# Performance work log

Measured on AMD Instinct MI355X. Metric: run time of the kernel, lower is better.

## Reference

```python
import jax, jax.numpy as jnp
import numpy as np

B, D = 8192, 64


def _mlp(x, w1, b1, w2, b2):
    # Linear -> exact GELU (torch nn.GELU default) -> Linear
    h = jax.nn.gelu(x @ w1 + b1, approximate=False)
    return h @ w2 + b2


def setup_inputs() -> dict:
    key = jax.random.key(0)
    ks = jax.random.split(key, 16)
    def lin(k, fan_in, fan_out):
        return jax.random.normal(k, (fan_in, fan_out), jnp.float32) / np.sqrt(fan_in).astype(np.float32)
    inp = {"z": jax.random.normal(ks[0], (B, 81, D), jnp.float32)}
    for i, name in enumerate(["row", "col", "box"]):
        inp[f"{name}_w1"] = lin(ks[1 + 4 * i], 9 * D, D)
        inp[f"{name}_b1"] = jnp.zeros((D,), jnp.float32)
        inp[f"{name}_w2"] = lin(ks[2 + 4 * i], D, D)
        inp[f"{name}_b2"] = jnp.zeros((D,), jnp.float32)
    inp["gate_w"] = lin(ks[13], 3 * D, D)
    inp["gate_b"] = jnp.zeros((D,), jnp.float32)
    inp["alpha"] = jnp.float32(0.1)
    return inp


def reference(z, row_w1, row_b1, row_w2, row_b2,
              col_w1, col_b1, col_w2, col_b2,
              box_w1, box_b1, box_w2, box_b2,
              gate_w, gate_b, alpha):
    Bv = z.shape[0]
    z_grid = z.reshape(Bv, 9, 9, D)
    # row context: each of 9 rows flattened -> (B, 9, 9D)
    row_ctx = z_grid.reshape(Bv, 9, 9 * D)
    row_up = _mlp(row_ctx, row_w1, row_b1, row_w2, row_b2)[:, :, None, :]  # (B,9,1,D)
    # col context: transpose rows/cols then flatten -> (B, 9, 9D)
    col_ctx = jnp.transpose(z_grid, (0, 2, 1, 3)).reshape(Bv, 9, 9 * D)
    col_up = _mlp(col_ctx, col_w1, col_b1, col_w2, col_b2)[:, None, :, :]  # (B,1,9,D)
    # box context: (B,3,3,3,3,D) -> (B, br, bc, r, c, D) -> (B, 9, 9D)
    box_ctx = jnp.transpose(z_grid.reshape(Bv, 3, 3, 3, 3, D), (0, 1, 3, 2, 4, 5)).reshape(Bv, 9, 9 * D)
    box_up = _mlp(box_ctx, box_w1, box_b1, box_w2, box_b2).reshape(Bv, 3, 3, D)
    # replicate exact torch expand+reshape semantics (mixes d and inner-col axes)
    box_up = jnp.broadcast_to(box_up[:, :, :, None, :, None], (Bv, 3, 3, 3, D, 3)).reshape(Bv, 9, 9, D)
    row_upb = jnp.broadcast_to(row_up, (Bv, 9, 9, D))
    col_upb = jnp.broadcast_to(col_up, (Bv, 9, 9, D))
    delta_sum = row_upb + col_upb + box_up
    gate_in = jnp.concatenate([row_upb, col_upb, box_up], axis=-1)  # (B,9,9,3D)
    gate = jax.nn.sigmoid(gate_in @ gate_w + gate_b)  # (B,9,9,D)
    z_new = z_grid + alpha * gate * delta_sum
    return z_new.reshape(Bv, 81, D)
```

## Files before the change

### kernel.cpp

```cpp
#include <hip/hip_runtime.h>
#include <hip/hip_bf16.h>

typedef __attribute__((ext_vector_type(8))) short short8;
typedef __attribute__((ext_vector_type(4))) short short4v;
typedef __attribute__((ext_vector_type(4))) float f32x4;

__device__ __forceinline__ unsigned short f2bf(float f) {
    union { __hip_bfloat16 b; unsigned short u; } v;
    v.b = __float2bfloat16(f);
    return v.u;
}
__device__ __forceinline__ float bf2f(unsigned short u) {
    return __uint_as_float(((unsigned)u) << 16);
}
__device__ __forceinline__ float gelu_tanh(float x) {
    float u = 0.79788456080286536f * x * (1.0f + 0.044715f * x * x);
    return x * __builtin_amdgcn_rcpf(1.0f + __builtin_exp2f(-2.8853900817779268f * u));
}
__device__ __forceinline__ float sigmoidf(float x) {
    return __builtin_amdgcn_rcpf(1.0f + __builtin_exp2f(-1.4426950408889634f * x));
}
__device__ __forceinline__ int swz(int row, int col) {
    return (row * 64 + col) ^ ((row & 7) << 3);
}

__global__ __launch_bounds__(256)
void prepack_kernel(const float* __restrict__ w1r, const float* __restrict__ w1c,
                    const float* __restrict__ w1b,
                    const float* __restrict__ w2r, const float* __restrict__ w2c,
                    const float* __restrict__ w2b,
                    const float* __restrict__ gw, unsigned short* __restrict__ ws)
{
    int t = blockIdx.x * 256 + threadIdx.x;
    if (t < 13824) {
        int wi = t / 4608, r = t % 4608;
        const float* src = (wi == 0) ? w1r : (wi == 1) ? w1c : w1b;
        unsigned short* dst = ws + wi * 36864;
        int lane = r & 63;
        int col = ((r >> 6) & 3) * 16 + (lane & 15);
        int k0 = (r >> 8) * 32 + (lane >> 4) * 8;
        #pragma unroll
        for (int j = 0; j < 8; ++j) dst[r * 8 + j] = f2bf(src[(k0 + j) * 64 + col]);
    } else if (t < 15360) {
        int q = t - 13824, wi = q / 512, r = q % 512;
        const float* src = (wi == 0) ? w2r : (wi == 1) ? w2c : w2b;
        unsigned short* dst = ws + 110592 + wi * 4096;
        int lane = r & 63;
        int col = ((r >> 6) & 3) * 16 + (lane & 15);
        int k0 = (r >> 8) * 32 + (lane >> 4) * 8;
        #pragma unroll
        for (int j = 0; j < 8; ++j) dst[r * 8 + j] = f2bf(src[(k0 + j) * 64 + col]);
    } else if (t < 17920) {
        int r = t - 15360;
        unsigned short* dst = ws + 122880;
        int lane = r & 63;
        int col = ((r >> 6) & 3) * 16 + (lane & 15);
        int k0 = (r >> 8) * 32 + (lane >> 4) * 8;
        #pragma unroll
        for (int j = 0; j < 8; ++j) {
            int krow = k0 + j;
            float v;
            if (krow < 128) {
                v = gw[krow * 64 + col];
            } else {
                int c = (krow - 128) >> 6, e = (krow - 128) & 63;
                int lo = 3 * e - 64 * c;
                v = 0.f;
                #pragma unroll
                for (int s = 0; s < 3; ++s) {
                    int dp = lo + s;
                    if (dp >= 0 && dp < 64) v += gw[(128 + dp) * 64 + col];
                }
            }
            dst[r * 8 + j] = f2bf(v);
        }
    }
}

#define UPWS_OFF 147456

__global__ __launch_bounds__(576, 2)
void k1_mlp(const float* __restrict__ z,
            const float* __restrict__ b1r, const float* __restrict__ b2r,
            const float* __restrict__ b1c, const float* __restrict__ b2c,
            const float* __restrict__ b1b, const float* __restrict__ b2b,
            const short* __restrict__ wsp, unsigned short* __restrict__ upws)
{
    __shared__ __align__(16) unsigned short zl[20736];
    __shared__ __align__(16) unsigned short hlds[9216];
    const int t = threadIdx.x;
    const int lane = t & 63;
    const int w = t >> 6;
    const int rl = lane & 15;
    const int kg = lane >> 4;
    const int b0 = blockIdx.x * 4;
    const int hoff = w * 1024;

    {
        const float* src = z + (size_t)b0 * 5184;
        #pragma unroll
        for (int it = 0; it < 9; ++it) {
            int g = t + it * 576;
            float4 v = *(const float4*)(src + g * 4);
            int row = g >> 4;
            int col = (g & 15) * 4;
            uint2 pk;
            pk.x = ((unsigned)f2bf(v.y) << 16) | f2bf(v.x);
            pk.y = ((unsigned)f2bf(v.w) << 16) | f2bf(v.z);
            *(uint2*)&zl[swz(row, col)] = pk;
        }
    }
    __syncthreads();

    const int type = w / 3, pg = w % 3;
    const int b = rl & 3, js = rl >> 2;
    const int jraw = 4 * pg + js;
    const int j = (jraw < 9) ? jraw : 8;
    const int cellbase = (type == 0) ? j * 9
                       : (type == 1) ? j
                       :               (j / 3) * 27 + (j % 3) * 3;
    const int rowbase = b * 81 + cellbase;

    const short* w1p = wsp + type * 36864;
    const short* w2p = wsp + 110592 + type * 4096;
    const float* b1p = (type == 0) ? b1r : (type == 1) ? b1c : b1b;
    const float* b2p = (type == 0) ? b2r : (type == 1) ? b2c : b2b;
    float b1v[4], b2v[4];
    #pragma unroll
    for (int nt = 0; nt < 4; ++nt) { b1v[nt] = b1p[nt * 16 + rl]; b2v[nt] = b2p[nt * 16 + rl]; }

    f32x4 acc[4];
    #pragma unroll
    for (int nt = 0; nt < 4; ++nt) acc[nt] = (f32x4)0.f;

    #pragma unroll
    for (int kk = 0; kk < 18; ++kk) {
        const int s = kk >> 1;
        const int sadd = (type == 0) ? s : (type == 1) ? 9 * s : (s / 3) * 9 + (s % 3);
        const int feat = (kk & 1) * 32 + kg * 8;
        short8 a = *(const short8*)&zl[swz(rowbase + sadd, feat)];
        #pragma unroll
        for (int nt = 0; nt < 4; ++nt) {
            short8 bv = *(const short8*)(w1p + ((kk * 4 + nt) * 64 + lane) * 8);
            acc[nt] = __builtin_amdgcn_mfma_f32_16x16x32_bf16(a, bv, acc[nt], 0, 0, 0);
        }
    }

    #pragma unroll
    for (int nt = 0; nt < 4; ++nt)
        #pragma unroll
        for (int reg = 0; reg < 4; ++reg)
            hlds[hoff + swz(kg * 4 + reg, nt * 16 + rl)] =
                f2bf(gelu_tanh(acc[nt][reg] + b1v[nt]));
    asm volatile("s_waitcnt lgkmcnt(0)" ::: "memory");

    f32x4 a2c[4];
    #pragma unroll
    for (int nt = 0; nt < 4; ++nt) a2c[nt] = (f32x4)0.f;
    #pragma unroll
    for (int kk2 = 0; kk2 < 2; ++kk2) {
        short8 a2 = *(const short8*)&hlds[hoff + swz(rl, kk2 * 32 + kg * 8)];
        #pragma unroll
        for (int nt = 0; nt < 4; ++nt) {
            short8 bw = *(const short8*)(w2p + ((kk2 * 4 + nt) * 64 + lane) * 8);
            a2c[nt] = __builtin_amdgcn_mfma_f32_16x16x32_bf16(a2, bw, a2c[nt], 0, 0, 0);
        }
    }
    asm volatile("s_waitcnt lgkmcnt(0)" ::: "memory");
    #pragma unroll
    for (int nt = 0; nt < 4; ++nt)
        #pragma unroll
        for (int reg = 0; reg < 4; ++reg)
            hlds[hoff + swz(kg * 4 + reg, nt * 16 + rl)] = f2bf(a2c[nt][reg] + b2v[nt]);
    asm volatile("s_waitcnt lgkmcnt(0)" ::: "memory");

    #pragma unroll
    for (int p2 = 0; p2 < 2; ++p2) {
        const int hrow = p2 * 8 + (lane >> 3), f0 = (lane & 7) * 8;
        const int sjs = hrow >> 2, sb = hrow & 3;
        const int sj = 4 * pg + sjs;
        if (sj < 9) {
            short8 v = *(const short8*)&hlds[hoff + swz(hrow, f0)];
            *(short8*)(upws + ((size_t)(b0 + sb) * 27 + type * 9 + sj) * 64 + f0) = v;
        }
    }
}

__global__ __launch_bounds__(576, 4)
void k2_gate(const float* __restrict__ z, const unsigned short* __restrict__ upws,
             const short* __restrict__ wsp, const float* __restrict__ gb,
             const float* __restrict__ alphap, float* __restrict__ out)
{
    __shared__ __align__(16) unsigned short ups[27648];
    __shared__ __align__(16) unsigned short tscr[9][1024];
    const int t = threadIdx.x;
    const int lane = t & 63;
    const int w = t >> 6;
    const int rl = lane & 15;
    const int kg = lane >> 4;
    const int b0 = blockIdx.x * 16;

    #pragma unroll
    for (int c6 = 0; c6 < 6; ++c6) {
        int chunk = t + c6 * 576;
        int row = chunk >> 3, f0 = (chunk & 7) * 8;
        short8 v = *(const short8*)(upws + (size_t)b0 * 1728 + chunk * 8);
        *(short8*)&ups[swz(row, f0)] = v;
    }
    __syncthreads();

    const short* gwp = wsp + 122880;
    const float alpha = alphap[0];
    float gbl[4][4];
    #pragma unroll
    for (int mt = 0; mt < 4; ++mt)
        #pragma unroll
        for (int reg = 0; reg < 4; ++reg) gbl[mt][reg] = gb[mt * 16 + kg * 4 + reg];

    const int c = w % 3, wg = w / 3;

    #pragma unroll
    for (int tl = 0; tl < 9; ++tl) {
        int e = (wg * 9 + tl) * 16 + rl;
        int b = e / 27, rem = e % 27, R = rem / 3, q = rem % 3, C = c + 3 * q;
        int rowR = b * 27 + R, rowC = b * 27 + 9 + C, rowB = b * 27 + 18 + R;

        f32x4 acc[4];
        #pragma unroll
        for (int mt = 0; mt < 4; ++mt) acc[mt] = (f32x4)0.f;

        #pragma unroll
        for (int s6 = 0; s6 < 6; ++s6) {
            int seg = s6 >> 1;
            int kkp = (s6 < 4) ? s6 : 4 + 2 * c + (s6 - 4);
            int row = (seg == 0) ? rowR : (seg == 1) ? rowC : rowB;
            int f = (s6 & 1) * 32 + kg * 8;
            short8 bfrag = *(const short8*)&ups[swz(row, f)];
            #pragma unroll
            for (int mt = 0; mt < 4; ++mt) {
                short8 afrag = *(const short8*)(gwp + ((kkp * 4 + mt) * 64 + lane) * 8);
                acc[mt] = __builtin_amdgcn_mfma_f32_16x16x32_bf16(afrag, bfrag, acc[mt], 0, 0, 0);
            }
        }

        #pragma unroll
        for (int mt = 0; mt < 4; ++mt) {
            short4v du4 = *(const short4v*)&ups[swz(rowR, mt * 16 + kg * 4)];
            short4v dc4 = *(const short4v*)&ups[swz(rowC, mt * 16 + kg * 4)];
            #pragma unroll
            for (int reg = 0; reg < 4; ++reg) {
                int fidx = mt * 16 + kg * 4 + reg;
                float g = sigmoidf(acc[mt][reg] + gbl[mt][reg]);
                float duv = bf2f((unsigned short)du4[reg]);
                float dcv = bf2f((unsigned short)dc4[reg]);
                float dbv = bf2f(ups[swz(rowB, (64 * c + fidx) / 3)]);
                tscr[w][swz(rl, fidx)] = f2bf(alpha * g * (duv + dcv + dbv));
            }
        }
        asm volatile("s_waitcnt lgkmcnt(0)" ::: "memory");
        #pragma unroll
        for (int p = 0; p < 2; ++p) {
            int cl = p * 8 + (lane >> 3), f0 = (lane & 7) * 8;
            int e2 = (wg * 9 + tl) * 16 + cl;
            int b2 = e2 / 27, rem2 = e2 % 27, R2 = rem2 / 3, C2 = c + 3 * (rem2 % 3);
            short8 tv = *(const short8*)&tscr[w][swz(cl, f0)];
            const float* zp = z + (size_t)(b0 + b2) * 5184 + (size_t)(R2 * 9 + C2) * 64 + f0;
            float4 z0 = *(const float4*)zp;
            float4 z1 = *(const float4*)(zp + 4);
            float4 o0, o1;
            o0.x = z0.x + bf2f((unsigned short)tv[0]);
            o0.y = z0.y + bf2f((unsigned short)tv[1]);
            o0.z = z0.z + bf2f((unsigned short)tv[2]);
            o0.w = z0.w + bf2f((unsigned short)tv[3]);
            o1.x = z1.x + bf2f((unsigned short)tv[4]);
            o1.y = z1.y + bf2f((unsigned short)tv[5]);
            o1.z = z1.z + bf2f((unsigned short)tv[6]);
            o1.w = z1.w + bf2f((unsigned short)tv[7]);
            float* op = out + (size_t)(b0 + b2) * 5184 + (size_t)(R2 * 9 + C2) * 64 + f0;
            *(float4*)op = o0;
            *(float4*)(op + 4) = o1;
        }
        asm volatile("s_waitcnt lgkmcnt(0)" ::: "memory");
    }
}

extern "C" void kernel_launch(void* const* d_in, const int* in_sizes, int n_in,
                              void* d_out, int out_size, void* d_ws, size_t ws_size,
                              hipStream_t stream) {
    const float* z   = (const float*)d_in[0];
    const float* w1r = (const float*)d_in[1];
    const float* b1r = (const float*)d_in[2];
    const float* w2r = (const float*)d_in[3];
    const float* b2r = (const float*)d_in[4];
    const float* w1c = (const float*)d_in[5];
    const float* b1c = (const float*)d_in[6];
    const float* w2c = (const float*)d_in[7];
    const float* b2c = (const float*)d_in[8];
    const float* w1b = (const float*)d_in[9];
    const float* b1b = (const float*)d_in[10];
    const float* w2b = (const float*)d_in[11];
    const float* b2b = (const float*)d_in[12];
    const float* gw  = (const float*)d_in[13];
    const float* gb  = (const float*)d_in[14];
    const float* al  = (const float*)d_in[15];
    float* outp = (float*)d_out;
    unsigned short* ws = (unsigned short*)d_ws;

    prepack_kernel<<<70, 256, 0, stream>>>(w1r, w1c, w1b, w2r, w2c, w2b, gw, ws);

    const int Btot = in_sizes[0] / 5184;
    unsigned short* upws = ws + UPWS_OFF;
    k1_mlp<<<Btot / 4, 576, 0, stream>>>(z, b1r, b2r, b1c, b2c, b1b, b2b,
                                         (const short*)ws, upws);
    k2_gate<<<Btot / 16, 576, 0, stream>>>(z, upws, (const short*)ws, gb, al, outp);
}
```

Before: 184.8 us.

## Fuse MLP and gate kernels into one kernel keeping updates in LDS

Merges the two-kernel pipeline (MLP writing bf16 row/col/box updates to a global workspace, then a gate kernel reading them back) into a single kernel per 4-batch block. The updates stay in shared memory and the gate stage reuses the hlds scratch, dropping the workspace round-trip and one launch. In exchange the gate stage now runs with 12 of 16 MFMA rows active per tile and at the MLP kernel's lower occupancy bound of 2 blocks. LDS use per block also grows.

```diff
diff --git a/kernel.cpp b/kernel.cpp
--- a/kernel.cpp
+++ b/kernel.cpp
@@ -77,16 +77,17 @@
     }
 }
 
-#define UPWS_OFF 147456
-
 __global__ __launch_bounds__(576, 2)
-void k1_mlp(const float* __restrict__ z,
-            const float* __restrict__ b1r, const float* __restrict__ b2r,
-            const float* __restrict__ b1c, const float* __restrict__ b2c,
-            const float* __restrict__ b1b, const float* __restrict__ b2b,
-            const short* __restrict__ wsp, unsigned short* __restrict__ upws)
+void fused_kernel(const float* __restrict__ z,
+                  const float* __restrict__ b1r, const float* __restrict__ b2r,
+                  const float* __restrict__ b1c, const float* __restrict__ b2c,
+                  const float* __restrict__ b1b, const float* __restrict__ b2b,
+                  const float* __restrict__ gb, const float* __restrict__ alphap,
+                  const short* __restrict__ wsp,
+                  float* __restrict__ out)
 {
     __shared__ __align__(16) unsigned short zl[20736];
+    __shared__ __align__(16) unsigned short ups[6912];
     __shared__ __align__(16) unsigned short hlds[9216];
     const int t = threadIdx.x;
     const int lane = t & 63;
@@ -112,175 +113,161 @@
     }
     __syncthreads();
 
-    const int type = w / 3, pg = w % 3;
-    const int b = rl & 3, js = rl >> 2;
-    const int jraw = 4 * pg + js;
-    const int j = (jraw < 9) ? jraw : 8;
-    const int cellbase = (type == 0) ? j * 9
-                       : (type == 1) ? j
-                       :               (j / 3) * 27 + (j % 3) * 3;
-    const int rowbase = b * 81 + cellbase;
-
-    const short* w1p = wsp + type * 36864;
-    const short* w2p = wsp + 110592 + type * 4096;
-    const float* b1p = (type == 0) ? b1r : (type == 1) ? b1c : b1b;
-    const float* b2p = (type == 0) ? b2r : (type == 1) ? b2c : b2b;
-    float b1v[4], b2v[4];
-    #pragma unroll
-    for (int nt = 0; nt < 4; ++nt) { b1v[nt] = b1p[nt * 16 + rl]; b2v[nt] = b2p[nt * 16 + rl]; }
-
-    f32x4 acc[4];
-    #pragma unroll
-    for (int nt = 0; nt < 4; ++nt) acc[nt] = (f32x4)0.f;
-
-    #pragma unroll
-    for (int kk = 0; kk < 18; ++kk) {
-        const int s = kk >> 1;
-        const int sadd = (type == 0) ? s : (type == 1) ? 9 * s : (s / 3) * 9 + (s % 3);
-        const int feat = (kk & 1) * 32 + kg * 8;
-        short8 a = *(const short8*)&zl[swz(rowbase + sadd, feat)];
-        #pragma unroll
-        for (int nt = 0; nt < 4; ++nt) {
-            short8 bv = *(const short8*)(w1p + ((kk * 4 + nt) * 64 + lane) * 8);
-            acc[nt] = __builtin_amdgcn_mfma_f32_16x16x32_bf16(a, bv, acc[nt], 0, 0, 0);
-        }
-    }
-
-    #pragma unroll
-    for (int nt = 0; nt < 4; ++nt)
-        #pragma unroll
-        for (int reg = 0; reg < 4; ++reg)
-            hlds[hoff + swz(kg * 4 + reg, nt * 16 + rl)] =
-                f2bf(gelu_tanh(acc[nt][reg] + b1v[nt]));
-    asm volatile("s_waitcnt lgkmcnt(0)" ::: "memory");
-
-    f32x4 a2c[4];
-    #pragma unroll
-    for (int nt = 0; nt < 4; ++nt) a2c[nt] = (f32x4)0.f;
-    #pragma unroll
-    for (int kk2 = 0; kk2 < 2; ++kk2) {
-        short8 a2 = *(const short8*)&hlds[hoff + swz(rl, kk2 * 32 + kg * 8)];
-        #pragma unroll
-        for (int nt = 0; nt < 4; ++nt) {
-            short8 bw = *(const short8*)(w2p + ((kk2 * 4 + nt) * 64 + lane) * 8);
-            a2c[nt] = __builtin_amdgcn_mfma_f32_16x16x32_bf16(a2, bw, a2c[nt], 0, 0, 0);
-        }
-    }
-    asm volatile("s_waitcnt lgkmcnt(0)" ::: "memory");
-    #pragma unroll
-    for (int nt = 0; nt < 4; ++nt)
-        #pragma unroll
-        for (int reg = 0; reg < 4; ++reg)
-            hlds[hoff + swz(kg * 4 + reg, nt * 16 + rl)] = f2bf(a2c[nt][reg] + b2v[nt]);
-    asm volatile("s_waitcnt lgkmcnt(0)" ::: "memory");
-
-    #pragma unroll
-    for (int p2 = 0; p2 < 2; ++p2) {
-        const int hrow = p2 * 8 + (lane >> 3), f0 = (lane & 7) * 8;
-        const int sjs = hrow >> 2, sb = hrow & 3;
-        const int sj = 4 * pg + sjs;
-        if (sj < 9) {
-            short8 v = *(const short8*)&hlds[hoff + swz(hrow, f0)];
-            *(short8*)(upws + ((size_t)(b0 + sb) * 27 + type * 9 + sj) * 64 + f0) = v;
-        }
-    }
-}
-
-__global__ __launch_bounds__(576, 4)
-void k2_gate(const float* __restrict__ z, const unsigned short* __restrict__ upws,
-             const short* __restrict__ wsp, const float* __restrict__ gb,
-             const float* __restrict__ alphap, float* __restrict__ out)
-{
-    __shared__ __align__(16) unsigned short ups[27648];
-    __shared__ __align__(16) unsigned short tscr[9][1024];
-    const int t = threadIdx.x;
-    const int lane = t & 63;
-    const int w = t >> 6;
-    const int rl = lane & 15;
-    const int kg = lane >> 4;
-    const int b0 = blockIdx.x * 16;
-
-    #pragma unroll
-    for (int c6 = 0; c6 < 6; ++c6) {
-        int chunk = t + c6 * 576;
-        int row = chunk >> 3, f0 = (chunk & 7) * 8;
-        short8 v = *(const short8*)(upws + (size_t)b0 * 1728 + chunk * 8);
-        *(short8*)&ups[swz(row, f0)] = v;
+    {
+        const int type = w / 3, pg = w % 3;
+        const int b = rl & 3, js = rl >> 2;
+        const int jraw = 4 * pg + js;
+        const int j = (jraw < 9) ? jraw : 8;
+        const int cellbase = (type == 0) ? j * 9
+                           : (type == 1) ? j
+                           :               (j / 3) * 27 + (j % 3) * 3;
+        const int rowbase = b * 81 + cellbase;
+
+        const short* w1p = wsp + type * 36864;
+        const short* w2p = wsp + 110592 + type * 4096;
+        const float* b1p = (type == 0) ? b1r : (type == 1) ? b1c : b1b;
+        const float* b2p = (type == 0) ? b2r : (type == 1) ? b2c : b2b;
+        float b1v[4], b2v[4];
+        #pragma unroll
+        for (int nt = 0; nt < 4; ++nt) { b1v[nt] = b1p[nt * 16 + rl]; b2v[nt] = b2p[nt * 16 + rl]; }
+
+        f32x4 acc[4];
+        #pragma unroll
+        for (int nt = 0; nt < 4; ++nt) acc[nt] = (f32x4)0.f;
+
+        #pragma unroll
+        for (int kk = 0; kk < 18; ++kk) {
+            const int s = kk >> 1;
+            const int sadd = (type == 0) ? s : (type == 1) ? 9 * s : (s / 3) * 9 + (s % 3);
+            const int feat = (kk & 1) * 32 + kg * 8;
+            short8 a = *(const short8*)&zl[swz(rowbase + sadd, feat)];
+            #pragma unroll
+            for (int nt = 0; nt < 4; ++nt) {
+                short8 bv = *(const short8*)(w1p + ((kk * 4 + nt) * 64 + lane) * 8);
+                acc[nt] = __builtin_amdgcn_mfma_f32_16x16x32_bf16(a, bv, acc[nt], 0, 0, 0);
+            }
+        }
+
+        #pragma unroll
+        for (int nt = 0; nt < 4; ++nt)
+            #pragma unroll
+            for (int reg = 0; reg < 4; ++reg)
+                hlds[hoff + swz(kg * 4 + reg, nt * 16 + rl)] =
+                    f2bf(gelu_tanh(acc[nt][reg] + b1v[nt]));
+        asm volatile("s_waitcnt lgkmcnt(0)" ::: "memory");
+
+        f32x4 a2c[4];
+        #pragma unroll
+        for (int nt = 0; nt < 4; ++nt) a2c[nt] = (f32x4)0.f;
+        #pragma unroll
+        for (int kk2 = 0; kk2 < 2; ++kk2) {
+            short8 a2 = *(const short8*)&hlds[hoff + swz(rl, kk2 * 32 + kg * 8)];
+            #pragma unroll
+            for (int nt = 0; nt < 4; ++nt) {
+                short8 bw = *(const short8*)(w2p + ((kk2 * 4 + nt) * 64 + lane) * 8);
+                a2c[nt] = __builtin_amdgcn_mfma_f32_16x16x32_bf16(a2, bw, a2c[nt], 0, 0, 0);
+            }
+        }
+        asm volatile("s_waitcnt lgkmcnt(0)" ::: "memory");
+        #pragma unroll
+        for (int nt = 0; nt < 4; ++nt)
+            #pragma unroll
+            for (int reg = 0; reg < 4; ++reg)
+                hlds[hoff + swz(kg * 4 + reg, nt * 16 + rl)] = f2bf(a2c[nt][reg] + b2v[nt]);
+        asm volatile("s_waitcnt lgkmcnt(0)" ::: "memory");
+
+        #pragma unroll
+        for (int p2 = 0; p2 < 2; ++p2) {
+            const int hrow = p2 * 8 + (lane >> 3), f0 = (lane & 7) * 8;
+            const int sjs = hrow >> 2, sb = hrow & 3;
+            const int sj = 4 * pg + sjs;
+            if (sj < 9) {
+                short8 v = *(const short8*)&hlds[hoff + swz(hrow, f0)];
+                *(short8*)&ups[swz(sb * 27 + type * 9 + sj, f0)] = v;
+            }
+        }
     }
     __syncthreads();
 
-    const short* gwp = wsp + 122880;
-    const float alpha = alphap[0];
-    float gbl[4][4];
-    #pragma unroll
-    for (int mt = 0; mt < 4; ++mt)
-        #pragma unroll
-        for (int reg = 0; reg < 4; ++reg) gbl[mt][reg] = gb[mt * 16 + kg * 4 + reg];
-
-    const int c = w % 3, wg = w / 3;
-
-    #pragma unroll
-    for (int tl = 0; tl < 9; ++tl) {
-        int e = (wg * 9 + tl) * 16 + rl;
-        int b = e / 27, rem = e % 27, R = rem / 3, q = rem % 3, C = c + 3 * q;
-        int rowR = b * 27 + R, rowC = b * 27 + 9 + C, rowB = b * 27 + 18 + R;
-
-        f32x4 acc[4];
-        #pragma unroll
-        for (int mt = 0; mt < 4; ++mt) acc[mt] = (f32x4)0.f;
-
-        #pragma unroll
-        for (int s6 = 0; s6 < 6; ++s6) {
-            int seg = s6 >> 1;
-            int kkp = (s6 < 4) ? s6 : 4 + 2 * c + (s6 - 4);
-            int row = (seg == 0) ? rowR : (seg == 1) ? rowC : rowB;
-            int f = (s6 & 1) * 32 + kg * 8;
-            short8 bfrag = *(const short8*)&ups[swz(row, f)];
+    {
+        const short* gwp = wsp + 122880;
+        const float alpha = alphap[0];
+        float gbl[4][4];
+        #pragma unroll
+        for (int mt = 0; mt < 4; ++mt)
+            #pragma unroll
+            for (int reg = 0; reg < 4; ++reg) gbl[mt][reg] = gb[mt * 16 + kg * 4 + reg];
+
+        const int c = w % 3, wg = w / 3;
+
+        #pragma unroll
+        for (int ti = 0; ti < 3; ++ti) {
+            const int ebase = wg * 36 + ti * 12;
+            const int el = (rl < 12) ? rl : 11;
+            int e = ebase + el;
+            int b = e / 27, rem = e % 27, R = rem / 3, q = rem % 3, C = c + 3 * q;
+            int rowR = b * 27 + R, rowC = b * 27 + 9 + C, rowB = b * 27 + 18 + R;
+
+            f32x4 acc[4];
+            #pragma unroll
+            for (int mt = 0; mt < 4; ++mt) acc[mt] = (f32x4)0.f;
+
+            #pragma unroll
+            for (int s6 = 0; s6 < 6; ++s6) {
+                int seg = s6 >> 1;
+                int kkp = (s6 < 4) ? s6 : 4 + 2 * c + (s6 - 4);
+                int row = (seg == 0) ? rowR : (seg == 1) ? rowC : rowB;
+                int f = (s6 & 1) * 32 + kg * 8;
+                short8 bfrag = *(const short8*)&ups[swz(row, f)];
+                #pragma unroll
+                for (int mt = 0; mt < 4; ++mt) {
+                    short8 afrag = *(const short8*)(gwp + ((kkp * 4 + mt) * 64 + lane) * 8);
+                    acc[mt] = __builtin_amdgcn_mfma_f32_16x16x32_bf16(afrag, bfrag, acc[mt], 0, 0, 0);
+                }
+            }
+
             #pragma unroll
             for (int mt = 0; mt < 4; ++mt) {
-                short8 afrag = *(const short8*)(gwp + ((kkp * 4 + mt) * 64 + lane) * 8);
-                acc[mt] = __builtin_amdgcn_mfma_f32_16x16x32_bf16(afrag, bfrag, acc[mt], 0, 0, 0);
-            }
-        }
-
-        #pragma unroll
-        for (int mt = 0; mt < 4; ++mt) {
-            short4v du4 = *(const short4v*)&ups[swz(rowR, mt * 16 + kg * 4)];
-            short4v dc4 = *(const short4v*)&ups[swz(rowC, mt * 16 + kg * 4)];
-            #pragma unroll
-            for (int reg = 0; reg < 4; ++reg) {
-                int fidx = mt * 16 + kg * 4 + reg;
-                float g = sigmoidf(acc[mt][reg] + gbl[mt][reg]);
-                float duv = bf2f((unsigned short)du4[reg]);
-                float dcv = bf2f((unsigned short)dc4[reg]);
-                float dbv = bf2f(ups[swz(rowB, (64 * c + fidx) / 3)]);
-                tscr[w][swz(rl, fidx)] = f2bf(alpha * g * (duv + dcv + dbv));
-            }
-        }
-        asm volatile("s_waitcnt lgkmcnt(0)" ::: "memory");
-        #pragma unroll
-        for (int p = 0; p < 2; ++p) {
-            int cl = p * 8 + (lane >> 3), f0 = (lane & 7) * 8;
-            int e2 = (wg * 9 + tl) * 16 + cl;
-            int b2 = e2 / 27, rem2 = e2 % 27, R2 = rem2 / 3, C2 = c + 3 * (rem2 % 3);
-            short8 tv = *(const short8*)&tscr[w][swz(cl, f0)];
-            const float* zp = z + (size_t)(b0 + b2) * 5184 + (size_t)(R2 * 9 + C2) * 64 + f0;
-            float4 z0 = *(const float4*)zp;
-            float4 z1 = *(const float4*)(zp + 4);
-            float4 o0, o1;
-            o0.x = z0.x + bf2f((unsigned short)tv[0]);
-            o0.y = z0.y + bf2f((unsigned short)tv[1]);
-            o0.z = z0.z + bf2f((unsigned short)tv[2]);
-            o0.w = z0.w + bf2f((unsigned short)tv[3]);
-            o1.x = z1.x + bf2f((unsigned short)tv[4]);
-            o1.y = z1.y + bf2f((unsigned short)tv[5]);
-            o1.z = z1.z + bf2f((unsigned short)tv[6]);
-            o1.w = z1.w + bf2f((unsigned short)tv[7]);
-            float* op = out + (size_t)(b0 + b2) * 5184 + (size_t)(R2 * 9 + C2) * 64 + f0;
-            *(float4*)op = o0;
-            *(float4*)(op + 4) = o1;
-        }
-        asm volatile("s_waitcnt lgkmcnt(0)" ::: "memory");
+                short4v du4 = *(const short4v*)&ups[swz(rowR, mt * 16 + kg * 4)];
+                short4v dc4 = *(const short4v*)&ups[swz(rowC, mt * 16 + kg * 4)];
+                #pragma unroll
+                for (int reg = 0; reg < 4; ++reg) {
+                    int fidx = mt * 16 + kg * 4 + reg;
+                    float g = sigmoidf(acc[mt][reg] + gbl[mt][reg]);
+                    float duv = bf2f((unsigned short)du4[reg]);
+                    float dcv = bf2f((unsigned short)dc4[reg]);
+                    float dbv = bf2f(ups[swz(rowB, (64 * c + fidx) / 3)]);
+                    hlds[hoff + swz(rl, fidx)] = f2bf(alpha * g * (duv + dcv + dbv));
+                }
+            }
+            asm volatile("s_waitcnt lgkmcnt(0)" ::: "memory");
+
+            #pragma unroll
+            for (int p = 0; p < 2; ++p) {
+                int cl = p * 8 + (lane >> 3), f0 = (lane & 7) * 8;
+                if (cl < 12) {
+                    int e2 = ebase + cl;
+                    int b2 = e2 / 27, rem2 = e2 % 27, R2 = rem2 / 3, C2 = c + 3 * (rem2 % 3);
+                    short8 tv = *(const short8*)&hlds[hoff + swz(cl, f0)];
+                    const float* zp = z + (size_t)(b0 + b2) * 5184 + (size_t)(R2 * 9 + C2) * 64 + f0;
+                    float4 z0 = *(const float4*)zp;
+                    float4 z1 = *(const float4*)(zp + 4);
+                    float4 o0, o1;
+                    o0.x = z0.x + bf2f((unsigned short)tv[0]);
+                    o0.y = z0.y + bf2f((unsigned short)tv[1]);
+                    o0.z = z0.z + bf2f((unsigned short)tv[2]);
+                    o0.w = z0.w + bf2f((unsigned short)tv[3]);
+                    o1.x = z1.x + bf2f((unsigned short)tv[4]);
+                    o1.y = z1.y + bf2f((unsigned short)tv[5]);
+                    o1.z = z1.z + bf2f((unsigned short)tv[6]);
+                    o1.w = z1.w + bf2f((unsigned short)tv[7]);
+                    float* op = out + (size_t)(b0 + b2) * 5184 + (size_t)(R2 * 9 + C2) * 64 + f0;
+                    *(float4*)op = o0;
+                    *(float4*)(op + 4) = o1;
+                }
+            }
+            asm volatile("s_waitcnt lgkmcnt(0)" ::: "memory");
+        }
     }
 }
 
@@ -309,8 +296,6 @@
     prepack_kernel<<<70, 256, 0, stream>>>(w1r, w1c, w1b, w2r, w2c, w2b, gw, ws);
 
     const int Btot = in_sizes[0] / 5184;
-    unsigned short* upws = ws + UPWS_OFF;
-    k1_mlp<<<Btot / 4, 576, 0, stream>>>(z, b1r, b2r, b1c, b2c, b1b, b2b,
-                                         (const short*)ws, upws);
-    k2_gate<<<Btot / 16, 576, 0, stream>>>(z, upws, (const short*)ws, gb, al, outp);
-}
+    fused_kernel<<<Btot / 4, 576, 0, stream>>>(
+        z, b1r, b2r, b1c, b2c, b1b, b2b, gb, al, (const short*)ws, outp);
+}
```

Result: slower. 203.5 us (+10.1%).

## Repartition first MLP GEMM across 12 waves by output column quarter

Applied to the files above, without the earlier changes.

The first-layer GEMM in k1_mlp is remapped so that each of 12 waves (768 threads) owns one MLP type and one 16-column quarter of the output, and computes three row groups. Each weight fragment loaded from global memory is then reused across three MFMAs instead of one, with three A-fragment LDS reads per step. The second layer keeps the old 9-wave mapping and runs after a block-wide barrier. In exchange the block is larger, there is an extra __syncthreads, and three waves sit idle during the second layer.

```diff
diff --git a/kernel.cpp b/kernel.cpp
--- a/kernel.cpp
+++ b/kernel.cpp
@@ -79,7 +79,7 @@
 
 #define UPWS_OFF 147456
 
-__global__ __launch_bounds__(576, 2)
+__global__ __launch_bounds__(768, 2)
 void k1_mlp(const float* __restrict__ z,
             const float* __restrict__ b1r, const float* __restrict__ b2r,
             const float* __restrict__ b1c, const float* __restrict__ b2c,
@@ -94,13 +94,10 @@
     const int rl = lane & 15;
     const int kg = lane >> 4;
     const int b0 = blockIdx.x * 4;
-    const int hoff = w * 1024;
 
     {
         const float* src = z + (size_t)b0 * 5184;
-        #pragma unroll
-        for (int it = 0; it < 9; ++it) {
-            int g = t + it * 576;
+        for (int g = t; g < 5184; g += 768) {
             float4 v = *(const float4*)(src + g * 4);
             int row = g >> 4;
             int col = (g & 15) * 4;
@@ -112,76 +109,85 @@
     }
     __syncthreads();
 
-    const int type = w / 3, pg = w % 3;
+    const int T = w >> 2, nq = w & 3;
+    const short* w1p = wsp + T * 36864;
+    const float* b1p = (T == 0) ? b1r : (T == 1) ? b1c : b1b;
+    const float b1s = b1p[nq * 16 + rl];
+
     const int b = rl & 3, js = rl >> 2;
-    const int jraw = 4 * pg + js;
-    const int j = (jraw < 9) ? jraw : 8;
-    const int cellbase = (type == 0) ? j * 9
-                       : (type == 1) ? j
-                       :               (j / 3) * 27 + (j % 3) * 3;
-    const int rowbase = b * 81 + cellbase;
-
-    const short* w1p = wsp + type * 36864;
-    const short* w2p = wsp + 110592 + type * 4096;
-    const float* b1p = (type == 0) ? b1r : (type == 1) ? b1c : b1b;
-    const float* b2p = (type == 0) ? b2r : (type == 1) ? b2c : b2b;
-    float b1v[4], b2v[4];
-    #pragma unroll
-    for (int nt = 0; nt < 4; ++nt) { b1v[nt] = b1p[nt * 16 + rl]; b2v[nt] = b2p[nt * 16 + rl]; }
-
-    f32x4 acc[4];
-    #pragma unroll
-    for (int nt = 0; nt < 4; ++nt) acc[nt] = (f32x4)0.f;
+    int rb0, rb1, rb2;
+    {
+        int j0 = 0 * 4 + js;  j0 = (j0 < 9) ? j0 : 8;
+        int j1 = 1 * 4 + js;  j1 = (j1 < 9) ? j1 : 8;
+        int j2 = 2 * 4 + js;  j2 = (j2 < 9) ? j2 : 8;
+        int c0 = (T == 0) ? j0 * 9 : (T == 1) ? j0 : (j0 / 3) * 27 + (j0 % 3) * 3;
+        int c1 = (T == 0) ? j1 * 9 : (T == 1) ? j1 : (j1 / 3) * 27 + (j1 % 3) * 3;
+        int c2 = (T == 0) ? j2 * 9 : (T == 1) ? j2 : (j2 / 3) * 27 + (j2 % 3) * 3;
+        rb0 = b * 81 + c0; rb1 = b * 81 + c1; rb2 = b * 81 + c2;
+    }
+
+    f32x4 acc0 = (f32x4)0.f, acc1 = (f32x4)0.f, acc2 = (f32x4)0.f;
 
     #pragma unroll
     for (int kk = 0; kk < 18; ++kk) {
         const int s = kk >> 1;
-        const int sadd = (type == 0) ? s : (type == 1) ? 9 * s : (s / 3) * 9 + (s % 3);
+        const int sadd = (T == 0) ? s : (T == 1) ? 9 * s : (s / 3) * 9 + (s % 3);
         const int feat = (kk & 1) * 32 + kg * 8;
-        short8 a = *(const short8*)&zl[swz(rowbase + sadd, feat)];
-        #pragma unroll
-        for (int nt = 0; nt < 4; ++nt) {
-            short8 bv = *(const short8*)(w1p + ((kk * 4 + nt) * 64 + lane) * 8);
-            acc[nt] = __builtin_amdgcn_mfma_f32_16x16x32_bf16(a, bv, acc[nt], 0, 0, 0);
-        }
-    }
-
-    #pragma unroll
-    for (int nt = 0; nt < 4; ++nt)
-        #pragma unroll
-        for (int reg = 0; reg < 4; ++reg)
-            hlds[hoff + swz(kg * 4 + reg, nt * 16 + rl)] =
-                f2bf(gelu_tanh(acc[nt][reg] + b1v[nt]));
-    asm volatile("s_waitcnt lgkmcnt(0)" ::: "memory");
-
-    f32x4 a2c[4];
-    #pragma unroll
-    for (int nt = 0; nt < 4; ++nt) a2c[nt] = (f32x4)0.f;
-    #pragma unroll
-    for (int kk2 = 0; kk2 < 2; ++kk2) {
-        short8 a2 = *(const short8*)&hlds[hoff + swz(rl, kk2 * 32 + kg * 8)];
-        #pragma unroll
-        for (int nt = 0; nt < 4; ++nt) {
-            short8 bw = *(const short8*)(w2p + ((kk2 * 4 + nt) * 64 + lane) * 8);
-            a2c[nt] = __builtin_amdgcn_mfma_f32_16x16x32_bf16(a2, bw, a2c[nt], 0, 0, 0);
-        }
-    }
-    asm volatile("s_waitcnt lgkmcnt(0)" ::: "memory");
-    #pragma unroll
-    for (int nt = 0; nt < 4; ++nt)
-        #pragma unroll
-        for (int reg = 0; reg < 4; ++reg)
-            hlds[hoff + swz(kg * 4 + reg, nt * 16 + rl)] = f2bf(a2c[nt][reg] + b2v[nt]);
-    asm volatile("s_waitcnt lgkmcnt(0)" ::: "memory");
-
-    #pragma unroll
-    for (int p2 = 0; p2 < 2; ++p2) {
-        const int hrow = p2 * 8 + (lane >> 3), f0 = (lane & 7) * 8;
-        const int sjs = hrow >> 2, sb = hrow & 3;
-        const int sj = 4 * pg + sjs;
-        if (sj < 9) {
-            short8 v = *(const short8*)&hlds[hoff + swz(hrow, f0)];
-            *(short8*)(upws + ((size_t)(b0 + sb) * 27 + type * 9 + sj) * 64 + f0) = v;
+        short8 bv = *(const short8*)(w1p + ((kk * 4 + nq) * 64 + lane) * 8);
+        short8 a0 = *(const short8*)&zl[swz(rb0 + sadd, feat)];
+        short8 a1 = *(const short8*)&zl[swz(rb1 + sadd, feat)];
+        short8 a2 = *(const short8*)&zl[swz(rb2 + sadd, feat)];
+        acc0 = __builtin_amdgcn_mfma_f32_16x16x32_bf16(a0, bv, acc0, 0, 0, 0);
+        acc1 = __builtin_amdgcn_mfma_f32_16x16x32_bf16(a1, bv, acc1, 0, 0, 0);
+        acc2 = __builtin_amdgcn_mfma_f32_16x16x32_bf16(a2, bv, acc2, 0, 0, 0);
+    }
+
+    #pragma unroll
+    for (int reg = 0; reg < 4; ++reg) {
+        hlds[(T * 3 + 0) * 1024 + swz(kg * 4 + reg, nq * 16 + rl)] = f2bf(gelu_tanh(acc0[reg] + b1s));
+        hlds[(T * 3 + 1) * 1024 + swz(kg * 4 + reg, nq * 16 + rl)] = f2bf(gelu_tanh(acc1[reg] + b1s));
+        hlds[(T * 3 + 2) * 1024 + swz(kg * 4 + reg, nq * 16 + rl)] = f2bf(gelu_tanh(acc2[reg] + b1s));
+    }
+    __syncthreads();
+
+    if (w < 9) {
+        const int T2 = w / 3, pg2 = w % 3;
+        const int hoff = w * 1024;
+        const short* w2p = wsp + 110592 + T2 * 4096;
+        const float* b2p = (T2 == 0) ? b2r : (T2 == 1) ? b2c : b2b;
+        float b2v[4];
+        #pragma unroll
+        for (int nt = 0; nt < 4; ++nt) b2v[nt] = b2p[nt * 16 + rl];
+
+        f32x4 a2c[4];
+        #pragma unroll
+        for (int nt = 0; nt < 4; ++nt) a2c[nt] = (f32x4)0.f;
+        #pragma unroll
+        for (int kk2 = 0; kk2 < 2; ++kk2) {
+            short8 a2 = *(const short8*)&hlds[hoff + swz(rl, kk2 * 32 + kg * 8)];
+            #pragma unroll
+            for (int nt = 0; nt < 4; ++nt) {
+                short8 bw = *(const short8*)(w2p + ((kk2 * 4 + nt) * 64 + lane) * 8);
+                a2c[nt] = __builtin_amdgcn_mfma_f32_16x16x32_bf16(a2, bw, a2c[nt], 0, 0, 0);
+            }
+        }
+        asm volatile("s_waitcnt lgkmcnt(0)" ::: "memory");
+        #pragma unroll
+        for (int nt = 0; nt < 4; ++nt)
+            #pragma unroll
+            for (int reg = 0; reg < 4; ++reg)
+                hlds[hoff + swz(kg * 4 + reg, nt * 16 + rl)] = f2bf(a2c[nt][reg] + b2v[nt]);
+        asm volatile("s_waitcnt lgkmcnt(0)" ::: "memory");
+
+        #pragma unroll
+        for (int p2 = 0; p2 < 2; ++p2) {
+            const int hrow = p2 * 8 + (lane >> 3), f0 = (lane & 7) * 8;
+            const int sjs = hrow >> 2, sb = hrow & 3;
+            const int sj = 4 * pg2 + sjs;
+            if (sj < 9) {
+                short8 v = *(const short8*)&hlds[hoff + swz(hrow, f0)];
+                *(short8*)(upws + ((size_t)(b0 + sb) * 27 + T2 * 9 + sj) * 64 + f0) = v;
+            }
         }
     }
 }
@@ -310,7 +316,7 @@
 
     const int Btot = in_sizes[0] / 5184;
     unsigned short* upws = ws + UPWS_OFF;
-    k1_mlp<<<Btot / 4, 576, 0, stream>>>(z, b1r, b2r, b1c, b2c, b1b, b2b,
+    k1_mlp<<<Btot / 4, 768, 0, stream>>>(z, b1r, b2r, b1c, b2c, b1b, b2b,
                                          (const short*)ws, upws);
     k2_gate<<<Btot / 16, 576, 0, stream>>>(z, upws, (const short*)ws, gb, al, outp);
 }
```

New measurement: 162.7 us, median of 2. -12.0%, faster.
